# Kernel optimization log

Hardware: AMD Instinct MI355X
Metric: run time of the kernel (lower is better)

## Reference

```python
import jax, jax.numpy as jnp
import numpy as np

B, S, C, H = 2, 2048, 1280, 20
D = C // H  # head_dim = 64


def setup_inputs() -> dict:
    key = jax.random.key(0)
    ks = jax.random.split(key, 5)
    scale = 1.0 / np.sqrt(C)
    return {
        "hidden_states": jax.random.normal(ks[0], (B, S, C), dtype=jnp.float32),
        "Wq": jax.random.normal(ks[1], (C, C), dtype=jnp.float32) * scale,
        "Wk": jax.random.normal(ks[2], (C, C), dtype=jnp.float32) * scale,
        "Wv": jax.random.normal(ks[3], (C, C), dtype=jnp.float32) * scale,
        "Wo": jax.random.normal(ks[4], (C, C), dtype=jnp.float32) * scale,
        "bo": jnp.zeros((C,), dtype=jnp.float32),
    }


def reference(hidden_states, Wq, Wk, Wv, Wo, bo):
    residual = hidden_states
    # q/k/v projections (self-attention: encoder_hidden_states is None)
    q = hidden_states @ Wq  # [B,S,C]
    k = hidden_states @ Wk
    v = hidden_states @ Wv
    # split heads -> [B,H,S,D]
    q = q.reshape(B, S, H, D).transpose(0, 2, 1, 3)
    k = k.reshape(B, S, H, D).transpose(0, 2, 1, 3)
    v = v.reshape(B, S, H, D).transpose(0, 2, 1, 3)
    scale = 1.0 / np.sqrt(D)
    scores = jnp.einsum('bhqd,bhkd->bhqk', q, k) * scale  # [B,H,S,S]
    attn_probs = jax.nn.softmax(scores, axis=-1)
    # loss term: Frobenius norm of the full attention-prob tensor (fp32)
    loss = jnp.sqrt(jnp.sum(jnp.square(attn_probs.astype(jnp.float32))))
    out = jnp.einsum('bhqk,bhkd->bhqd', attn_probs, v)  # [B,H,S,D]
    out = out.transpose(0, 2, 1, 3).reshape(B, S, C)
    out = out @ Wo + bo
    out = out + residual  # residual_connection=True, rescale_output_factor=1.0
    return out, loss
```

## Files before the change

kernel.cpp:

```cpp
#include <hip/hip_runtime.h>
#include <hip/hip_bf16.h>
#include <math.h>

#define B_SZ   2
#define S_LEN  2048
#define C_DIM  1280
#define H_NUM  20
#define D_HEAD 64
#define M_TOT  (B_SZ * S_LEN)

typedef __bf16 bf16;
typedef __bf16 bf16x8 __attribute__((ext_vector_type(8)));
typedef __bf16 bf16x4 __attribute__((ext_vector_type(4)));
typedef float  f32x4  __attribute__((ext_vector_type(4)));

__device__ inline f32x4 zero4() { f32x4 z; z[0]=z[1]=z[2]=z[3]=0.f; return z; }

__device__ __forceinline__ void async_copy16(void* lds, const void* g) {
    __builtin_amdgcn_global_load_lds(
        (const __attribute__((address_space(1))) unsigned int*)g,
        (__attribute__((address_space(3))) unsigned int*)lds,
        16, 0, 0);
}

__global__ __launch_bounds__(256) void k_convert_hs(const float* __restrict__ in,
                                                    bf16* __restrict__ out) {
    int i = (blockIdx.x * 256 + threadIdx.x) * 4;
    float4 v = *(const float4*)(in + i);
    bf16x4 o; o[0]=(bf16)v.x; o[1]=(bf16)v.y; o[2]=(bf16)v.z; o[3]=(bf16)v.w;
    *(bf16x4*)(out + i) = o;
}

__global__ __launch_bounds__(256) void k_transpose_w(
    const float* __restrict__ w0, const float* __restrict__ w1,
    const float* __restrict__ w2, const float* __restrict__ w3,
    bf16* __restrict__ o0, bf16* __restrict__ o1,
    bf16* __restrict__ o2, bf16* __restrict__ o3) {
    __shared__ float t[32][33];
    const float* w = blockIdx.z==0 ? w0 : blockIdx.z==1 ? w1 : blockIdx.z==2 ? w2 : w3;
    bf16*       o  = blockIdx.z==0 ? o0 : blockIdx.z==1 ? o1 : blockIdx.z==2 ? o2 : o3;
    int k0 = blockIdx.y*32, n0 = blockIdx.x*32;
    int tx = threadIdx.x & 31, ty = threadIdx.x >> 5;
    #pragma unroll
    for (int i = 0; i < 32; i += 8)
        t[ty+i][tx] = w[(size_t)(k0+ty+i)*C_DIM + n0 + tx];
    __syncthreads();
    #pragma unroll
    for (int i = 0; i < 32; i += 8)
        o[(size_t)(n0+ty+i)*C_DIM + k0 + tx] = (bf16)t[tx][ty+i];
}

#define QBM 256
#define QBN 256
#define QBK 32
#define QNT (C_DIM / QBK)
__global__ __launch_bounds__(512, 2) void k_gemm_qkv(
    const bf16* __restrict__ A,
    const bf16* __restrict__ Wcat,
    bf16* __restrict__ Qo, bf16* __restrict__ Ko, bf16* __restrict__ VTo) {
    __shared__ bf16 lds[3][2][QBM][QBK];
    const int m0  = blockIdx.y * QBM;
    const int nx  = blockIdx.x;
    const int z   = nx / 5;
    const int nw0 = (nx % 5) * QBN;
    const int ng0 = nx * QBN;
    const int tid = threadIdx.x, lane = tid & 63, wid = tid >> 6;
    const int wm = wid >> 2, wn = wid & 3;
    const int g = lane >> 4, lr = lane & 15;
    const float scale = (z==0) ? 0.18033688011112042f : 1.0f;

    f32x4 acc[8][4];
    #pragma unroll
    for (int i=0;i<8;i++)
        #pragma unroll
        for (int j=0;j<4;j++)
            acc[i][j] = zero4();

#define QSTAGE(bf, kt)                                                       \
    { const int k0_ = (kt)*QBK;                                              \
      _Pragma("unroll")                                                      \
      for (int c = 0; c < 2; ++c) {                                          \
        int p = c*512 + tid;                                                 \
        int row = p >> 2, gp = p & 3;                                        \
        async_copy16((char*)&lds[bf][0][0][0] + p*16,                        \
                     &A[(size_t)(m0+row)*C_DIM + k0_ + gp*8]);               \
        async_copy16((char*)&lds[bf][1][0][0] + p*16,                        \
                     &Wcat[(size_t)(ng0+row)*C_DIM + k0_ + gp*8]);           \
      } }

    QSTAGE(0, 0);
    QSTAGE(1, 1);
    asm volatile("s_waitcnt vmcnt(4)" ::: "memory");
    __builtin_amdgcn_s_barrier();

    int cur = 0;
    for (int t = 0; t < QNT; ++t) {
        if (t + 2 < QNT) {
            int sb = cur + 2; if (sb >= 3) sb -= 3;
            QSTAGE(sb, t + 2);
        }
        const bf16* AB = &lds[cur][0][0][0];
        const bf16* BB = &lds[cur][1][0][0];
        bf16x8 af[8], bfr[4];
        #pragma unroll
        for (int mf = 0; mf < 8; ++mf)
            af[mf] = *(const bf16x8*)(AB + (wm*128 + mf*16 + lr)*QBK + g*8);
        #pragma unroll
        for (int nf = 0; nf < 4; ++nf)
            bfr[nf] = *(const bf16x8*)(BB + (wn*64 + nf*16 + lr)*QBK + g*8);
        #pragma unroll
        for (int mf = 0; mf < 8; ++mf)
            #pragma unroll
            for (int nf = 0; nf < 4; ++nf)
                acc[mf][nf] = __builtin_amdgcn_mfma_f32_16x16x32_bf16(
                    af[mf], bfr[nf], acc[mf][nf], 0,0,0);
        if (t + 2 < QNT) asm volatile("s_waitcnt vmcnt(4) lgkmcnt(0)" ::: "memory");
        else             asm volatile("s_waitcnt vmcnt(0) lgkmcnt(0)" ::: "memory");
        __builtin_amdgcn_s_barrier();
        if (++cur == 3) cur = 0;
    }

    if (z == 2) {
        #pragma unroll
        for (int mf=0;mf<8;mf++) {
            #pragma unroll
            for (int nf=0;nf<4;nf++) {
                int n = nw0 + wn*64 + nf*16 + lr;
                int h = n >> 6, d = n & 63;
                int m = m0 + wm*128 + mf*16 + g*4;
                int b = m >> 11, s = m & (S_LEN-1);
                bf16x4 ov;
                #pragma unroll
                for (int r=0;r<4;r++) ov[r] = (bf16)acc[mf][nf][r];
                *(bf16x4*)&VTo[((size_t)(b*H_NUM + h)*D_HEAD + d)*S_LEN + s] = ov;
            }
        }
    } else {
        bf16* Out = (z==0) ? Qo : Ko;
        #pragma unroll
        for (int mf=0;mf<8;mf++) {
            #pragma unroll
            for (int nf=0;nf<4;nf++) {
                int n = nw0 + wn*64 + nf*16 + lr;
                int h = n >> 6, d = n & 63;
                #pragma unroll
                for (int r=0;r<4;r++) {
                    int m = m0 + wm*128 + mf*16 + g*4 + r;
                    int b = m >> 11, s = m & (S_LEN-1);
                    Out[(size_t)((b*H_NUM + h)*S_LEN + s)*D_HEAD + d] = (bf16)(acc[mf][nf][r] * scale);
                }
            }
        }
    }
}

#define BM 128
#define BN 128
#define BK 64

#define GEMM_STAGE(Al, Bl, Aptr, Bptr, m0, n0, k0)                                \
    {                                                                             \
        _Pragma("unroll")                                                         \
        for (int c = 0; c < 4; ++c) {                                             \
            int p = c*256 + tid;                                                  \
            int row = p >> 3, gp = p & 7, gc = gp ^ (row & 7);                    \
            async_copy16((char*)Al + p*16,                                        \
                         &Aptr[(size_t)((m0)+row)*C_DIM + (k0) + gc*8]);          \
            async_copy16((char*)Bl + p*16,                                        \
                         &Bptr[(size_t)((n0)+row)*C_DIM + (k0) + gc*8]);          \
        }                                                                         \
    }

#define GEMM_COMPUTE(Al, Bl)                                                      \
    {                                                                             \
        _Pragma("unroll")                                                         \
        for (int kk = 0; kk < 2; ++kk) {                                          \
            bf16x8 af[4], bfr[4];                                                 \
            _Pragma("unroll")                                                     \
            for (int mf = 0; mf < 4; ++mf) {                                      \
                int arow = wm*64 + mf*16 + lr;                                    \
                af[mf] = *(const bf16x8*)((char*)Al + arow*128 +                  \
                          (((kk*4 + g) ^ (arow & 7)) << 4));                      \
            }                                                                     \
            _Pragma("unroll")                                                     \
            for (int nf = 0; nf < 4; ++nf) {                                      \
                int brow = wn*64 + nf*16 + lr;                                    \
                bfr[nf] = *(const bf16x8*)((char*)Bl + brow*128 +                 \
                          (((kk*4 + g) ^ (brow & 7)) << 4));                      \
            }                                                                     \
            _Pragma("unroll")                                                     \
            for (int mf = 0; mf < 4; ++mf)                                        \
                _Pragma("unroll")                                                 \
                for (int nf = 0; nf < 4; ++nf)                                    \
                    acc[mf][nf] = __builtin_amdgcn_mfma_f32_16x16x32_bf16(        \
                        af[mf], bfr[nf], acc[mf][nf], 0,0,0);                     \
        }                                                                         \
    }

__global__ __launch_bounds__(256) void k_gemm_out(
    const bf16* __restrict__ A,
    const bf16* __restrict__ WoT,
    const float* __restrict__ bo,
    const float* __restrict__ res,
    float* __restrict__ out) {
    __shared__ bf16 Al[BM][BK];
    __shared__ bf16 Bl[BN][BK];
    const int m0 = blockIdx.y * BM, n0 = blockIdx.x * BN;
    const int tid = threadIdx.x, lane = tid & 63, wid = tid >> 6;
    const int wm = wid >> 1, wn = wid & 1;
    const int g = lane >> 4, lr = lane & 15;
    f32x4 acc[4][4];
    #pragma unroll
    for (int i=0;i<4;i++)
        #pragma unroll
        for (int j=0;j<4;j++)
            acc[i][j] = zero4();
    for (int k0 = 0; k0 < C_DIM; k0 += BK) {
        GEMM_STAGE(Al, Bl, A, WoT, m0, n0, k0);
        __syncthreads();
        GEMM_COMPUTE(Al, Bl);
        __syncthreads();
    }
    #pragma unroll
    for (int mf=0;mf<4;mf++) {
        #pragma unroll
        for (int nf=0;nf<4;nf++) {
            int n = n0 + wn*64 + nf*16 + lr;
            float bias = bo[n];
            #pragma unroll
            for (int r=0;r<4;r++) {
                int m = m0 + wm*64 + mf*16 + g*4 + r;
                size_t idx = (size_t)m*C_DIM + n;
                out[idx] = acc[mf][nf][r] + bias + res[idx];
            }
        }
    }
}

#define KVB 64
__global__ __launch_bounds__(256) void k_attn(
    const bf16* __restrict__ Q,
    const bf16* __restrict__ Kg,
    const bf16* __restrict__ VT,
    bf16* __restrict__ O,
    float* __restrict__ lossPart) {
    __shared__ bf16 Kl[2][KVB][64];
    __shared__ bf16 Vl[2][D_HEAD][64];

    const int id  = blockIdx.x;
    const int fid = (id & 7) * 160 + (id >> 3);
    const int bh = fid >> 5;
    const int qb = fid & 31;
    const int b = bh / H_NUM, hh = bh % H_NUM;
    const int tid = threadIdx.x, lane = tid & 63, wid = tid >> 6;
    const int g = lane >> 4, lr = lane & 15;

    const bf16* Kbase = Kg + (size_t)bh * S_LEN * D_HEAD;
    const bf16* Vbase = VT + (size_t)bh * D_HEAD * S_LEN;

    const int qrow = qb*64 + wid*16 + lr;
    const bf16* qp = Q + ((size_t)bh*S_LEN + qrow)*D_HEAD;
    const bf16x8 aq0 = *(const bf16x8*)(qp + g*8);
    const bf16x8 aq1 = *(const bf16x8*)(qp + 32 + g*8);

    bf16x8 ones;
    #pragma unroll
    for (int i=0;i<8;i++) ones[i] = (bf16)1.0f;

    const int lb7 = (lr & 3) | (((lr >> 2) & 1) << 2);
    const int lhi = ((lr >> 2) & 2) << 3;

    f32x4 o_acc[4];
    #pragma unroll
    for (int i=0;i<4;i++) o_acc[i] = zero4();
    f32x4 l_acc = zero4();
    f32x4 s2m   = zero4();

#define STAGE(buf, kv0)                                                          \
    {                                                                            \
        _Pragma("unroll")                                                        \
        for (int pp=0; pp<2; ++pp) {                                             \
            int p = pp*256 + tid;                                                \
            int lrow = p >> 3, gp = p & 7;                                       \
            int tl = (lrow & 51) | ((lrow & 4) << 1) | ((lrow & 8) >> 1);        \
            async_copy16((char*)&Kl[buf][0][0] + p*16,                           \
                         Kbase + (size_t)((kv0) + tl)*D_HEAD                     \
                               + ((gp ^ (lrow & 7)) << 3));                      \
        }                                                                        \
        _Pragma("unroll")                                                        \
        for (int pp=0; pp<2; ++pp) {                                             \
            int p = pp*256 + tid;                                                \
            int drow = p >> 3, gp = p & 7;                                       \
            async_copy16((char*)&Vl[buf][0][0] + p*16,                           \
                         Vbase + (size_t)drow*S_LEN + (kv0)                      \
                               + ((gp ^ (drow & 7)) << 3));                      \
        }                                                                        \
    }

    STAGE(0, 0);
    __syncthreads();

    for (int t = 0; t < S_LEN/KVB; ++t) {
        const int cur = t & 1;
        if (t + 1 < S_LEN/KVB) STAGE(cur^1, (t+1)*KVB);
        const bf16* KB = &Kl[cur][0][0];
        const bf16* VB = &Vl[cur][0][0];

        f32x4 accp[2][2];
        __builtin_amdgcn_s_setprio(1);
        #pragma unroll
        for (int pair=0; pair<2; ++pair)
            #pragma unroll
            for (int u=0; u<2; ++u) {
                const bf16* kr = KB + (pair*32 + (u<<3) + lhi + lb7)*64;
                bf16x8 k0 = *(const bf16x8*)(kr + ((g       ^ lb7) << 3));
                bf16x8 k1 = *(const bf16x8*)(kr + (((4 + g) ^ lb7) << 3));
                f32x4 c = zero4();
                c = __builtin_amdgcn_mfma_f32_16x16x32_bf16(k0, aq0, c, 0,0,0);
                c = __builtin_amdgcn_mfma_f32_16x16x32_bf16(k1, aq1, c, 0,0,0);
                accp[pair][u] = c;
            }
        __builtin_amdgcn_s_setprio(0);
        bf16x8 pb[2];
        #pragma unroll
        for (int pair=0; pair<2; ++pair)
            #pragma unroll
            for (int u=0; u<2; ++u)
                #pragma unroll
                for (int r=0; r<4; ++r) {
                    float e = __builtin_amdgcn_exp2f(accp[pair][u][r]);
                    pb[pair][u*4+r] = (bf16)e;
                }
        __builtin_amdgcn_s_setprio(1);
        l_acc = __builtin_amdgcn_mfma_f32_16x16x32_bf16(ones, pb[0], l_acc, 0,0,0);
        l_acc = __builtin_amdgcn_mfma_f32_16x16x32_bf16(ones, pb[1], l_acc, 0,0,0);
        s2m = __builtin_amdgcn_mfma_f32_16x16x32_bf16(pb[0], pb[0], s2m, 0,0,0);
        s2m = __builtin_amdgcn_mfma_f32_16x16x32_bf16(pb[1], pb[1], s2m, 0,0,0);
        #pragma unroll
        for (int ds_=0; ds_<4; ++ds_) {
            const bf16* vr = VB + (ds_*16 + lr)*64;
            #pragma unroll
            for (int pair=0; pair<2; ++pair) {
                bf16x8 v = *(const bf16x8*)(vr + (((pair*4 + g) ^ (lr & 7)) << 3));
                o_acc[ds_] = __builtin_amdgcn_mfma_f32_16x16x32_bf16(v, pb[pair], o_acc[ds_], 0,0,0);
            }
        }
        __builtin_amdgcn_s_setprio(0);
        __syncthreads();
    }

    const float lfull = l_acc[0];

    const float inv = 1.0f / lfull;
    bf16* orow = O + ((size_t)(b*S_LEN + qrow)*H_NUM + hh)*D_HEAD;
    #pragma unroll
    for (int ds_=0; ds_<4; ++ds_) {
        bf16x4 ov;
        #pragma unroll
        for (int r=0; r<4; ++r) ov[r] = (bf16)(o_acc[ds_][r] * inv);
        *(bf16x4*)(orow + ds_*16 + g*4) = ov;
    }
    float v = 0.f;
    if (g == (lr >> 2)) v = s2m[lr & 3] / (lfull * lfull);
    #pragma unroll
    for (int msk=1; msk<64; msk<<=1) v += __shfl_xor(v, msk);
    if (lane == 0) lossPart[(bh*32 + qb)*4 + wid] = v;
}

__global__ __launch_bounds__(256) void k_loss(const float* __restrict__ part,
                                              float* __restrict__ out, int n) {
    __shared__ float w[4];
    float s = 0.f;
    for (int i = threadIdx.x; i < n; i += 256) s += part[i];
    #pragma unroll
    for (int msk=1; msk<64; msk<<=1) s += __shfl_xor(s, msk);
    int lane = threadIdx.x & 63, wid = threadIdx.x >> 6;
    if (lane==0) w[wid] = s;
    __syncthreads();
    if (threadIdx.x==0) out[(size_t)M_TOT*C_DIM] = sqrtf(w[0]+w[1]+w[2]+w[3]);
}

extern "C" void kernel_launch(void* const* d_in, const int* in_sizes, int n_in,
                              void* d_out, int out_size, void* d_ws, size_t ws_size,
                              hipStream_t stream) {
    (void)in_sizes; (void)n_in; (void)out_size; (void)ws_size;
    const float* hs = (const float*)d_in[0];
    const float* Wq = (const float*)d_in[1];
    const float* Wk = (const float*)d_in[2];
    const float* Wv = (const float*)d_in[3];
    const float* Wo = (const float*)d_in[4];
    const float* bo = (const float*)d_in[5];
    float* out = (float*)d_out;

    constexpr size_t HS_E = (size_t)M_TOT * C_DIM;
    constexpr size_t W_E  = (size_t)C_DIM * C_DIM;
    char* ws = (char*)d_ws;
    size_t off = 0;
    bf16* hs_bf = (bf16*)(ws + off); off += HS_E * 2;
    bf16* WqT   = (bf16*)(ws + off); off += W_E * 2;
    bf16* WkT   = (bf16*)(ws + off); off += W_E * 2;
    bf16* WvT   = (bf16*)(ws + off); off += W_E * 2;
    bf16* WoT   = (bf16*)(ws + off); off += W_E * 2;
    bf16* Qb    = (bf16*)(ws + off); off += HS_E * 2;
    bf16* Kb    = (bf16*)(ws + off); off += HS_E * 2;
    bf16* Vtb   = (bf16*)(ws + off); off += HS_E * 2;
    bf16* Ob    = (bf16*)(ws + off); off += HS_E * 2;
    float* lossPart = (float*)(ws + off); off += 5120 * 4;

    k_convert_hs<<<HS_E/(256*4), 256, 0, stream>>>(hs, hs_bf);
    k_transpose_w<<<dim3(C_DIM/32, C_DIM/32, 4), 256, 0, stream>>>(Wq, Wk, Wv, Wo, WqT, WkT, WvT, WoT);
    k_gemm_qkv<<<dim3(3*C_DIM/QBN, M_TOT/QBM), 512, 0, stream>>>(hs_bf, WqT, Qb, Kb, Vtb);
    k_attn<<<1280, 256, 0, stream>>>(Qb, Kb, Vtb, Ob, lossPart);
    k_gemm_out<<<dim3(C_DIM/BN, M_TOT/BM), 256, 0, stream>>>(Ob, WoT, bo, hs, out);
    k_loss<<<1, 256, 0, stream>>>(lossPart, out, 5120);
}
```

Before: 175.3 us.

## Double-buffer output GEMM and process two query tiles per attention block

The output-projection GEMM now double-buffers its LDS tiles, issuing the async load of the next K slice before computing the current one. This replaces the stage-sync-compute-sync pattern and is meant to overlap global loads with MFMA work. The attention kernel now handles 128 query rows per block (two 64-row halves) instead of 64, so each staged K/V tile is reused twice, halving K/V LDS traffic and the block count. The cost is more accumulator registers per wave, possibly lower occupancy, and fewer blocks (640) to spread across CUs.

```diff
diff --git a/kernel.cpp b/kernel.cpp
--- a/kernel.cpp
+++ b/kernel.cpp
@@ -164,9 +164,9 @@
         for (int c = 0; c < 4; ++c) {                                             \
             int p = c*256 + tid;                                                  \
             int row = p >> 3, gp = p & 7, gc = gp ^ (row & 7);                    \
-            async_copy16((char*)Al + p*16,                                        \
+            async_copy16((char*)(Al) + p*16,                                      \
                          &Aptr[(size_t)((m0)+row)*C_DIM + (k0) + gc*8]);          \
-            async_copy16((char*)Bl + p*16,                                        \
+            async_copy16((char*)(Bl) + p*16,                                      \
                          &Bptr[(size_t)((n0)+row)*C_DIM + (k0) + gc*8]);          \
         }                                                                         \
     }
@@ -179,13 +179,13 @@
             _Pragma("unroll")                                                     \
             for (int mf = 0; mf < 4; ++mf) {                                      \
                 int arow = wm*64 + mf*16 + lr;                                    \
-                af[mf] = *(const bf16x8*)((char*)Al + arow*128 +                  \
+                af[mf] = *(const bf16x8*)((char*)(Al) + arow*128 +                \
                           (((kk*4 + g) ^ (arow & 7)) << 4));                      \
             }                                                                     \
             _Pragma("unroll")                                                     \
             for (int nf = 0; nf < 4; ++nf) {                                      \
                 int brow = wn*64 + nf*16 + lr;                                    \
-                bfr[nf] = *(const bf16x8*)((char*)Bl + brow*128 +                 \
+                bfr[nf] = *(const bf16x8*)((char*)(Bl) + brow*128 +               \
                           (((kk*4 + g) ^ (brow & 7)) << 4));                      \
             }                                                                     \
             _Pragma("unroll")                                                     \
@@ -203,8 +203,8 @@
     const float* __restrict__ bo,
     const float* __restrict__ res,
     float* __restrict__ out) {
-    __shared__ bf16 Al[BM][BK];
-    __shared__ bf16 Bl[BN][BK];
+    __shared__ bf16 Al[2][BM][BK];
+    __shared__ bf16 Bl[2][BN][BK];
     const int m0 = blockIdx.y * BM, n0 = blockIdx.x * BN;
     const int tid = threadIdx.x, lane = tid & 63, wid = tid >> 6;
     const int wm = wid >> 1, wn = wid & 1;
@@ -215,11 +215,17 @@
         #pragma unroll
         for (int j=0;j<4;j++)
             acc[i][j] = zero4();
+    GEMM_STAGE(&Al[0][0][0], &Bl[0][0][0], A, WoT, m0, n0, 0);
+    asm volatile("s_waitcnt vmcnt(0)" ::: "memory");
+    __builtin_amdgcn_s_barrier();
+    int cur = 0;
     for (int k0 = 0; k0 < C_DIM; k0 += BK) {
-        GEMM_STAGE(Al, Bl, A, WoT, m0, n0, k0);
-        __syncthreads();
-        GEMM_COMPUTE(Al, Bl);
-        __syncthreads();
+        if (k0 + BK < C_DIM)
+            GEMM_STAGE(&Al[cur^1][0][0], &Bl[cur^1][0][0], A, WoT, m0, n0, k0 + BK);
+        GEMM_COMPUTE(&Al[cur][0][0], &Bl[cur][0][0]);
+        asm volatile("s_waitcnt vmcnt(0) lgkmcnt(0)" ::: "memory");
+        __builtin_amdgcn_s_barrier();
+        cur ^= 1;
     }
     #pragma unroll
     for (int mf=0;mf<4;mf++) {
@@ -248,9 +254,9 @@
     __shared__ bf16 Vl[2][D_HEAD][64];
 
     const int id  = blockIdx.x;
-    const int fid = (id & 7) * 160 + (id >> 3);
-    const int bh = fid >> 5;
-    const int qb = fid & 31;
+    const int fid = (id & 7) * 80 + (id >> 3);
+    const int bh = fid >> 4;
+    const int qb = fid & 15;
     const int b = bh / H_NUM, hh = bh % H_NUM;
     const int tid = threadIdx.x, lane = tid & 63, wid = tid >> 6;
     const int g = lane >> 4, lr = lane & 15;
@@ -258,10 +264,15 @@
     const bf16* Kbase = Kg + (size_t)bh * S_LEN * D_HEAD;
     const bf16* Vbase = VT + (size_t)bh * D_HEAD * S_LEN;
 
-    const int qrow = qb*64 + wid*16 + lr;
-    const bf16* qp = Q + ((size_t)bh*S_LEN + qrow)*D_HEAD;
-    const bf16x8 aq0 = *(const bf16x8*)(qp + g*8);
-    const bf16x8 aq1 = *(const bf16x8*)(qp + 32 + g*8);
+    bf16x8 aq[2][2];
+    int qrow[2];
+    #pragma unroll
+    for (int h=0; h<2; ++h) {
+        qrow[h] = qb*128 + h*64 + wid*16 + lr;
+        const bf16* qp = Q + ((size_t)bh*S_LEN + qrow[h])*D_HEAD;
+        aq[h][0] = *(const bf16x8*)(qp + g*8);
+        aq[h][1] = *(const bf16x8*)(qp + 32 + g*8);
+    }
 
     bf16x8 ones;
     #pragma unroll
@@ -270,11 +281,14 @@
     const int lb7 = (lr & 3) | (((lr >> 2) & 1) << 2);
     const int lhi = ((lr >> 2) & 2) << 3;
 
-    f32x4 o_acc[4];
-    #pragma unroll
-    for (int i=0;i<4;i++) o_acc[i] = zero4();
-    f32x4 l_acc = zero4();
-    f32x4 s2m   = zero4();
+    f32x4 o_acc[2][4];
+    f32x4 l_acc[2], s2m[2];
+    #pragma unroll
+    for (int h=0;h<2;++h) {
+        #pragma unroll
+        for (int i=0;i<4;i++) o_acc[h][i] = zero4();
+        l_acc[h] = zero4(); s2m[h] = zero4();
+    }
 
 #define STAGE(buf, kv0)                                                          \
     {                                                                            \
@@ -306,7 +320,7 @@
         const bf16* KB = &Kl[cur][0][0];
         const bf16* VB = &Vl[cur][0][0];
 
-        f32x4 accp[2][2];
+        f32x4 accp[2][2][2];
         __builtin_amdgcn_s_setprio(1);
         #pragma unroll
         for (int pair=0; pair<2; ++pair)
@@ -315,56 +329,72 @@
                 const bf16* kr = KB + (pair*32 + (u<<3) + lhi + lb7)*64;
                 bf16x8 k0 = *(const bf16x8*)(kr + ((g       ^ lb7) << 3));
                 bf16x8 k1 = *(const bf16x8*)(kr + (((4 + g) ^ lb7) << 3));
-                f32x4 c = zero4();
-                c = __builtin_amdgcn_mfma_f32_16x16x32_bf16(k0, aq0, c, 0,0,0);
-                c = __builtin_amdgcn_mfma_f32_16x16x32_bf16(k1, aq1, c, 0,0,0);
-                accp[pair][u] = c;
+                #pragma unroll
+                for (int h=0; h<2; ++h) {
+                    f32x4 c = zero4();
+                    c = __builtin_amdgcn_mfma_f32_16x16x32_bf16(k0, aq[h][0], c, 0,0,0);
+                    c = __builtin_amdgcn_mfma_f32_16x16x32_bf16(k1, aq[h][1], c, 0,0,0);
+                    accp[h][pair][u] = c;
+                }
             }
         __builtin_amdgcn_s_setprio(0);
-        bf16x8 pb[2];
-        #pragma unroll
-        for (int pair=0; pair<2; ++pair)
-            #pragma unroll
-            for (int u=0; u<2; ++u)
+        bf16x8 pb[2][2];
+        #pragma unroll
+        for (int h=0; h<2; ++h)
+            #pragma unroll
+            for (int pair=0; pair<2; ++pair)
                 #pragma unroll
-                for (int r=0; r<4; ++r) {
-                    float e = __builtin_amdgcn_exp2f(accp[pair][u][r]);
-                    pb[pair][u*4+r] = (bf16)e;
-                }
+                for (int u=0; u<2; ++u)
+                    #pragma unroll
+                    for (int r=0; r<4; ++r) {
+                        float e = __builtin_amdgcn_exp2f(accp[h][pair][u][r]);
+                        pb[h][pair][u*4+r] = (bf16)e;
+                    }
         __builtin_amdgcn_s_setprio(1);
-        l_acc = __builtin_amdgcn_mfma_f32_16x16x32_bf16(ones, pb[0], l_acc, 0,0,0);
-        l_acc = __builtin_amdgcn_mfma_f32_16x16x32_bf16(ones, pb[1], l_acc, 0,0,0);
-        s2m = __builtin_amdgcn_mfma_f32_16x16x32_bf16(pb[0], pb[0], s2m, 0,0,0);
-        s2m = __builtin_amdgcn_mfma_f32_16x16x32_bf16(pb[1], pb[1], s2m, 0,0,0);
+        #pragma unroll
+        for (int h=0; h<2; ++h) {
+            l_acc[h] = __builtin_amdgcn_mfma_f32_16x16x32_bf16(ones, pb[h][0], l_acc[h], 0,0,0);
+            l_acc[h] = __builtin_amdgcn_mfma_f32_16x16x32_bf16(ones, pb[h][1], l_acc[h], 0,0,0);
+            s2m[h]   = __builtin_amdgcn_mfma_f32_16x16x32_bf16(pb[h][0], pb[h][0], s2m[h], 0,0,0);
+            s2m[h]   = __builtin_amdgcn_mfma_f32_16x16x32_bf16(pb[h][1], pb[h][1], s2m[h], 0,0,0);
+        }
         #pragma unroll
         for (int ds_=0; ds_<4; ++ds_) {
             const bf16* vr = VB + (ds_*16 + lr)*64;
             #pragma unroll
             for (int pair=0; pair<2; ++pair) {
                 bf16x8 v = *(const bf16x8*)(vr + (((pair*4 + g) ^ (lr & 7)) << 3));
-                o_acc[ds_] = __builtin_amdgcn_mfma_f32_16x16x32_bf16(v, pb[pair], o_acc[ds_], 0,0,0);
+                #pragma unroll
+                for (int h=0; h<2; ++h)
+                    o_acc[h][ds_] = __builtin_amdgcn_mfma_f32_16x16x32_bf16(v, pb[h][pair], o_acc[h][ds_], 0,0,0);
             }
         }
         __builtin_amdgcn_s_setprio(0);
         __syncthreads();
     }
 
-    const float lfull = l_acc[0];
-
-    const float inv = 1.0f / lfull;
-    bf16* orow = O + ((size_t)(b*S_LEN + qrow)*H_NUM + hh)*D_HEAD;
-    #pragma unroll
-    for (int ds_=0; ds_<4; ++ds_) {
-        bf16x4 ov;
-        #pragma unroll
-        for (int r=0; r<4; ++r) ov[r] = (bf16)(o_acc[ds_][r] * inv);
-        *(bf16x4*)(orow + ds_*16 + g*4) = ov;
+    float lfull[2];
+    #pragma unroll
+    for (int h=0; h<2; ++h) {
+        lfull[h] = l_acc[h][0];
+        const float inv = 1.0f / lfull[h];
+        bf16* orow = O + ((size_t)(b*S_LEN + qrow[h])*H_NUM + hh)*D_HEAD;
+        #pragma unroll
+        for (int ds_=0; ds_<4; ++ds_) {
+            bf16x4 ov;
+            #pragma unroll
+            for (int r=0; r<4; ++r) ov[r] = (bf16)(o_acc[h][ds_][r] * inv);
+            *(bf16x4*)(orow + ds_*16 + g*4) = ov;
+        }
     }
     float v = 0.f;
-    if (g == (lr >> 2)) v = s2m[lr & 3] / (lfull * lfull);
+    if (g == (lr >> 2)) {
+        v  = s2m[0][lr & 3] / (lfull[0] * lfull[0]);
+        v += s2m[1][lr & 3] / (lfull[1] * lfull[1]);
+    }
     #pragma unroll
     for (int msk=1; msk<64; msk<<=1) v += __shfl_xor(v, msk);
-    if (lane == 0) lossPart[(bh*32 + qb)*4 + wid] = v;
+    if (lane == 0) lossPart[(bh*16 + qb)*4 + wid] = v;
 }
 
 __global__ __launch_bounds__(256) void k_loss(const float* __restrict__ part,
@@ -405,12 +435,12 @@
     bf16* Kb    = (bf16*)(ws + off); off += HS_E * 2;
     bf16* Vtb   = (bf16*)(ws + off); off += HS_E * 2;
     bf16* Ob    = (bf16*)(ws + off); off += HS_E * 2;
-    float* lossPart = (float*)(ws + off); off += 5120 * 4;
+    float* lossPart = (float*)(ws + off); off += 2560 * 4;
 
     k_convert_hs<<<HS_E/(256*4), 256, 0, stream>>>(hs, hs_bf);
     k_transpose_w<<<dim3(C_DIM/32, C_DIM/32, 4), 256, 0, stream>>>(Wq, Wk, Wv, Wo, WqT, WkT, WvT, WoT);
     k_gemm_qkv<<<dim3(3*C_DIM/QBN, M_TOT/QBM), 512, 0, stream>>>(hs_bf, WqT, Qb, Kb, Vtb);
-    k_attn<<<1280, 256, 0, stream>>>(Qb, Kb, Vtb, Ob, lossPart);
+    k_attn<<<640, 256, 0, stream>>>(Qb, Kb, Vtb, Ob, lossPart);
     k_gemm_out<<<dim3(C_DIM/BN, M_TOT/BM), 256, 0, stream>>>(Ob, WoT, bo, hs, out);
-    k_loss<<<1, 256, 0, stream>>>(lossPart, out, 5120);
-}
+    k_loss<<<1, 256, 0, stream>>>(lossPart, out, 2560);
+}
```

New measurement: 181.5 us. 3.5% more time.
